# Kernel tuning notes

Hardware: AMD Instinct MI355X
Metric: run time of the kernel (lower is better)

## Reference

```python
import jax, jax.numpy as jnp
import numpy as np
import math

B, C, H, W = 8, 512, 32, 32
NUM_HEADS = 8          # channels // num_head_channels = 512 // 64
NUM_GROUPS = 32        # GroupNorm32
EPS = 1e-5


def setup_inputs() -> dict:
    key = jax.random.key(0)
    k1, k2, k3, k4, k5 = jax.random.split(key, 5)
    x = jax.random.normal(k1, (B, C, H, W), dtype=jnp.float32)
    # GroupNorm affine params (torch init: ones/zeros)
    norm_scale = jnp.ones((C,), dtype=jnp.float32)
    norm_bias = jnp.zeros((C,), dtype=jnp.float32)
    # 1x1 Conv1d weights: qkv maps C -> 3C, proj maps C -> C
    qkv_w = jax.random.normal(k2, (3 * C, C), dtype=jnp.float32) * 0.02
    qkv_b = jax.random.normal(k3, (3 * C,), dtype=jnp.float32) * 0.02
    # NOTE: original zero-inits proj_out; we use small random weights so the
    # block computes non-trivial math (same op structure, same FLOPs).
    proj_w = jax.random.normal(k4, (C, C), dtype=jnp.float32) * 0.02
    proj_b = jax.random.normal(k5, (C,), dtype=jnp.float32) * 0.02
    return {"x": x, "norm_scale": norm_scale, "norm_bias": norm_bias,
            "qkv_w": qkv_w, "qkv_b": qkv_b, "proj_w": proj_w, "proj_b": proj_b}


def _attention_block(x, norm_scale, norm_bias, qkv_w, qkv_b, proj_w, proj_b):
    b, c, h, w = x.shape
    t = h * w
    xf = x.reshape(b, c, t)
    # GroupNorm32: fp32 compute, 32 groups, biased variance, eps=1e-5
    g = xf.astype(jnp.float32).reshape(b, NUM_GROUPS, c // NUM_GROUPS, t)
    mean = g.mean(axis=(2, 3), keepdims=True)
    var = g.var(axis=(2, 3), keepdims=True)
    gn = ((g - mean) * jax.lax.rsqrt(var + EPS)).reshape(b, c, t)
    gn = (gn * norm_scale[None, :, None] + norm_bias[None, :, None]).astype(xf.dtype)
    # 1x1 conv == channel matmul: [B,C,T] -> [B,3C,T]
    qkv = jnp.einsum('oc,bct->bot', qkv_w, gn) + qkv_b[None, :, None]
    # Legacy head layout: [B, H*3*ch, T] -> [B*H, 3*ch, T]
    ch = c // NUM_HEADS
    qkv = qkv.reshape(b * NUM_HEADS, 3 * ch, t)
    q, k, v = jnp.split(qkv, 3, axis=1)          # each [B*H, ch, T]
    scale = 1.0 / math.sqrt(math.sqrt(ch))
    weight = jnp.einsum('bct,bcs->bts', q * scale, k * scale)  # [B*H, T, T]
    weight = jax.nn.softmax(weight.astype(jnp.float32), axis=-1).astype(qkv.dtype)
    a = jnp.einsum('bts,bcs->bct', weight, v).reshape(b, c, t)
    out = jnp.einsum('oc,bct->bot', proj_w, a) + proj_b[None, :, None]
    return (xf + out).reshape(b, c, h, w)


def reference(x, norm_scale, norm_bias, qkv_w, qkv_b, proj_w, proj_b):
    return _attention_block(x, norm_scale, norm_bias, qkv_w, qkv_b, proj_w, proj_b)
```

## Files before the change

kernel.cpp:

```cpp
#include <hip/hip_runtime.h>
#include <math.h>

#define B_   8
#define C_   512
#define T_   1024
#define G_   32
#define CPG  16
#define NH   8
#define OC3  1536
#define EPS  1e-5f

#define QSCALE 0.18033688011112042f
#define C_OFF  11.541560327111708f

typedef __bf16 bf16;
typedef __bf16 bf16x4 __attribute__((ext_vector_type(4)));
typedef __bf16 bf16x8 __attribute__((ext_vector_type(8)));
typedef float  f32x4  __attribute__((ext_vector_type(4)));
typedef short  s16x4  __attribute__((ext_vector_type(4)));

#define MFMA16(a, b, c) __builtin_amdgcn_mfma_f32_16x16x32_bf16((a), (b), (c), 0, 0, 0)

__device__ __forceinline__ f32x4 mfma_k16(bf16x4 a, bf16x4 b, f32x4 c) {
#if __has_builtin(__builtin_amdgcn_mfma_f32_16x16x16_bf16)
    return __builtin_amdgcn_mfma_f32_16x16x16_bf16(a, b, c, 0, 0, 0);
#else
    return __builtin_amdgcn_mfma_f32_16x16x16bf16_1k(
        __builtin_bit_cast(s16x4, a), __builtin_bit_cast(s16x4, b), c, 0, 0, 0);
#endif
}

__device__ __forceinline__ float fexp2(float x) {
#if defined(__has_builtin)
#if __has_builtin(__builtin_amdgcn_exp2f)
    return __builtin_amdgcn_exp2f(x);
#else
    return __expf(x * 0.6931471805599453f);
#endif
#else
    return __expf(x * 0.6931471805599453f);
#endif
}

__global__ __launch_bounds__(256) void cvt_both(const float* __restrict__ w1,
                                                bf16* __restrict__ wb1,
                                                const float* __restrict__ w2,
                                                bf16* __restrict__ wb2)
{
    int blk = blockIdx.x;
    const float* src = (blk < 768) ? w1 : w2;
    bf16* dst        = (blk < 768) ? wb1 : wb2;
    int i = (blk < 768 ? blk : blk - 768) * 256 + threadIdx.x;
    float4 v = ((const float4*)src)[i];
    bf16x4 o;
    o[0] = (bf16)v.x; o[1] = (bf16)v.y; o[2] = (bf16)v.z; o[3] = (bf16)v.w;
    *(bf16x4*)(dst + (size_t)i * 4) = o;
}

__global__ __launch_bounds__(256) void gn_kernel(const float* __restrict__ x,
                                                 const float* __restrict__ scale,
                                                 const float* __restrict__ bias,
                                                 bf16* __restrict__ gnT)
{
    const int blk = blockIdx.x;
    const int b = blk >> 5, g = blk & 31;
    const size_t base = (size_t)blk * (CPG * T_);
    const float4* xin = (const float4*)(x + base);
    const int tid = threadIdx.x;

    float s = 0.f, ss = 0.f;
    float4 vals[16];
#pragma unroll
    for (int i = 0; i < 16; ++i) {
        float4 v = xin[tid + i * 256];
        vals[i] = v;
        s  += v.x + v.y + v.z + v.w;
        ss += v.x * v.x + v.y * v.y + v.z * v.z + v.w * v.w;
    }

    __shared__ float rs[256], rss[256];
    rs[tid] = s; rss[tid] = ss;
    __syncthreads();
    for (int off = 128; off > 0; off >>= 1) {
        if (tid < off) { rs[tid] += rs[tid + off]; rss[tid] += rss[tid + off]; }
        __syncthreads();
    }
    const float invN = 1.f / (float)(CPG * T_);
    const float mean = rs[0] * invN;
    const float var  = rss[0] * invN - mean * mean;
    const float inv  = rsqrtf(var + EPS);

    const int c0 = g * CPG;
    float sc[16], bi[16];
#pragma unroll
    for (int i = 0; i < 16; ++i) {
        float s_ = scale[c0 + i] * inv;
        sc[i] = s_;
        bi[i] = bias[c0 + i] - mean * s_;
    }
    bf16* ob = gnT + (size_t)b * (T_ * C_) + c0;
#pragma unroll
    for (int tt = 0; tt < 4; ++tt) {
        bf16x8 lo, hi;
#pragma unroll
        for (int i = 0; i < 8; ++i) {
            float v0 = (tt == 0) ? vals[i].x : (tt == 1) ? vals[i].y
                     : (tt == 2) ? vals[i].z : vals[i].w;
            float v1 = (tt == 0) ? vals[i + 8].x : (tt == 1) ? vals[i + 8].y
                     : (tt == 2) ? vals[i + 8].z : vals[i + 8].w;
            lo[i] = (bf16)(v0 * sc[i] + bi[i]);
            hi[i] = (bf16)(v1 * sc[i + 8] + bi[i + 8]);
        }
        bf16* p = ob + (size_t)(4 * tid + tt) * C_;
        *(bf16x8*)p       = lo;
        *(bf16x8*)(p + 8) = hi;
    }
}

template <int MODE>
__global__ __launch_bounds__(256) void mm128(const bf16* __restrict__ Arows,
                                             const bf16* __restrict__ Wt,
                                             const float* __restrict__ bias,
                                             const float* __restrict__ x,
                                             void* __restrict__ outp)
{
    const int b   = blockIdx.z;
    const int o0  = blockIdx.y * 128;
    const int t0  = blockIdx.x * 128;
    const int tid = threadIdx.x;
    const int lane = tid & 63;
    const int w  = tid >> 6;
    const int wr = w >> 1, wc = w & 1;
    const int lq = lane & 15, lg = lane >> 4;

    __shared__ __align__(16) bf16 Ag[128][72];
    __shared__ __align__(16) bf16 Bg[128][72];

    const bf16* gA = Arows + (size_t)b * (T_ * C_) + (size_t)t0 * C_;
    const bf16* gB = Wt + (size_t)o0 * C_;

    f32x4 acc[4][4];
#pragma unroll
    for (int i = 0; i < 4; ++i)
#pragma unroll
        for (int j = 0; j < 4; ++j) { acc[i][j][0]=0.f; acc[i][j][1]=0.f; acc[i][j][2]=0.f; acc[i][j][3]=0.f; }

    bf16x8 areg[4], breg[4];
#pragma unroll
    for (int it = 0; it < 4; ++it) {
        int chunk = it * 256 + tid, row = chunk >> 3, cp = chunk & 7;
        areg[it] = *(const bf16x8*)(gA + (size_t)row * C_ + cp * 8);
        breg[it] = *(const bf16x8*)(gB + (size_t)row * C_ + cp * 8);
    }

    for (int k0 = 0; k0 < C_; k0 += 64) {
        __syncthreads();
#pragma unroll
        for (int it = 0; it < 4; ++it) {
            int chunk = it * 256 + tid, row = chunk >> 3, cp = chunk & 7;
            *(bf16x8*)&Ag[row][cp * 8] = areg[it];
            *(bf16x8*)&Bg[row][cp * 8] = breg[it];
        }
        __syncthreads();
        if (k0 + 64 < C_) {
#pragma unroll
            for (int it = 0; it < 4; ++it) {
                int chunk = it * 256 + tid, row = chunk >> 3, cp = chunk & 7;
                areg[it] = *(const bf16x8*)(gA + (size_t)row * C_ + k0 + 64 + cp * 8);
                breg[it] = *(const bf16x8*)(gB + (size_t)row * C_ + k0 + 64 + cp * 8);
            }
        }
#pragma unroll
        for (int kb = 0; kb < 2; ++kb) {
            bf16x8 af[4], bfr[4];
#pragma unroll
            for (int i = 0; i < 4; ++i) {
                af[i]  = *(const bf16x8*)&Ag[wr * 64 + i * 16 + lq][kb * 32 + lg * 8];
                bfr[i] = *(const bf16x8*)&Bg[wc * 64 + i * 16 + lq][kb * 32 + lg * 8];
            }
#pragma unroll
            for (int mf = 0; mf < 4; ++mf)
#pragma unroll
                for (int nf = 0; nf < 4; ++nf)
                    acc[mf][nf] = MFMA16(af[mf], bfr[nf], acc[mf][nf]);
        }
    }

    if (MODE == 0) {
        bf16* qkvT = (bf16*)outp;
#pragma unroll
        for (int nf = 0; nf < 4; ++nf) {
            int chg = o0 + wc * 64 + nf * 16 + lq;
            int seg = chg >> 6;
            int which = seg % 3;
            int chs = chg & 63;
            float bv = bias[chg];
            bf16* outb = qkvT + (size_t)(b * 24 + seg) * (T_ * 64);
            if (which != 2) {
                float osc = (which == 0) ? QSCALE : 1.0f;
#pragma unroll
                for (int mf = 0; mf < 4; ++mf) {
                    int tb = t0 + wr * 64 + mf * 16 + lg * 4;
#pragma unroll
                    for (int r = 0; r < 4; ++r)
                        outb[(size_t)(tb + r) * 64 + chs] = (bf16)((acc[mf][nf][r] + bv) * osc);
                }
            } else {
#pragma unroll
                for (int mf = 0; mf < 4; ++mf) {
                    int tb = t0 + wr * 64 + mf * 16 + lg * 4;
                    bf16x4 pb;
#pragma unroll
                    for (int r = 0; r < 4; ++r) pb[r] = (bf16)(acc[mf][nf][r] + bv);
                    *(bf16x4*)(outb + (size_t)chs * T_ + tb) = pb;
                }
            }
        }
    } else {
        float* out = (float*)outp;
#pragma unroll
        for (int nf = 0; nf < 4; ++nf) {
            int o = o0 + wc * 64 + nf * 16 + lq;
            float bv = bias[o];
#pragma unroll
            for (int mf = 0; mf < 4; ++mf) {
                int tb = t0 + wr * 64 + mf * 16 + lg * 4;
                size_t idx = ((size_t)b * C_ + o) * T_ + tb;
                float4 xr = *(const float4*)(x + idx);
                float4 rv;
                rv.x = acc[mf][nf][0] + bv + xr.x;
                rv.y = acc[mf][nf][1] + bv + xr.y;
                rv.z = acc[mf][nf][2] + bv + xr.z;
                rv.w = acc[mf][nf][3] + bv + xr.w;
                *(float4*)(out + idx) = rv;
            }
        }
    }
}

__global__ __launch_bounds__(256) void attn_kernel(const bf16* __restrict__ qkvT,
                                                   bf16* __restrict__ aT)
{
    const int id = blockIdx.x;
    const int bh = id & 63;
    const int tile = id >> 6;
    const int tid = threadIdx.x;
    const int lane = tid & 63;
    const int w  = tid >> 6;
    const int lq = lane & 15;
    const int lg = lane >> 4;
    const int q0 = tile * 128 + w * 32;

    const bf16* qb = qkvT + (size_t)(bh * 3 + 0) * (T_ * 64);
    const bf16* kb = qkvT + (size_t)(bh * 3 + 1) * (T_ * 64);
    const bf16* vb = qkvT + (size_t)(bh * 3 + 2) * (T_ * 64);

    __shared__ __align__(16) bf16 ks[64][72];
    __shared__ __align__(16) bf16 vs[64][136];

    bf16x8 qf[2][2];
#pragma unroll
    for (int qg = 0; qg < 2; ++qg)
#pragma unroll
        for (int kh = 0; kh < 2; ++kh)
            qf[qg][kh] = *(const bf16x8*)(qb + (size_t)(q0 + qg * 16 + lq) * 64 + kh * 32 + lg * 8);

    f32x4 oacc[2][4];
#pragma unroll
    for (int qg = 0; qg < 2; ++qg)
#pragma unroll
        for (int og = 0; og < 4; ++og) { oacc[qg][og][0]=0.f; oacc[qg][og][1]=0.f; oacc[qg][og][2]=0.f; oacc[qg][og][3]=0.f; }
    float lloc[2] = {0.f, 0.f};

    const int sr = tid >> 3, scp = tid & 7;
    bf16x8 kreg[2], vreg[2];
#pragma unroll
    for (int it = 0; it < 2; ++it) {
        kreg[it] = *(const bf16x8*)(kb + (size_t)(sr + it * 32) * 64 + scp * 8);
        vreg[it] = *(const bf16x8*)(vb + (size_t)(sr + it * 32) * T_ + scp * 8);
    }

    for (int s0 = 0; s0 < T_; s0 += 64) {
        __syncthreads();
#pragma unroll
        for (int it = 0; it < 2; ++it) {
            *(bf16x8*)&ks[sr + it * 32][scp * 8] = kreg[it];
            *(bf16x8*)&vs[sr + it * 32][scp * 8] = vreg[it];
        }
        __syncthreads();
        if (s0 + 64 < T_) {
            int sn = s0 + 64;
#pragma unroll
            for (int it = 0; it < 2; ++it) {
                kreg[it] = *(const bf16x8*)(kb + (size_t)(sn + sr + it * 32) * 64 + scp * 8);
                vreg[it] = *(const bf16x8*)(vb + (size_t)(sr + it * 32) * T_ + sn + scp * 8);
            }
        }

        f32x4 st[2][4];
        f32x4 cinit; cinit[0] = -C_OFF; cinit[1] = -C_OFF; cinit[2] = -C_OFF; cinit[3] = -C_OFF;
#pragma unroll
        for (int g = 0; g < 4; ++g) {
            bf16x8 kf0 = *(const bf16x8*)&ks[g * 16 + lq][lg * 8];
            bf16x8 kf1 = *(const bf16x8*)&ks[g * 16 + lq][32 + lg * 8];
#pragma unroll
            for (int qg = 0; qg < 2; ++qg) {
                st[qg][g] = MFMA16(kf0, qf[qg][0], cinit);
                st[qg][g] = MFMA16(kf1, qf[qg][1], st[qg][g]);
            }
        }
        bf16x4 pa16[2][4];
#pragma unroll
        for (int qg = 0; qg < 2; ++qg) {
            float ll = 0.f;
#pragma unroll
            for (int g = 0; g < 4; ++g) {
#pragma unroll
                for (int r = 0; r < 4; ++r) {
                    float p = fexp2(st[qg][g][r]);
                    ll += p;
                    pa16[qg][g][r] = (bf16)p;
                }
            }
            lloc[qg] += ll;
        }
#pragma unroll
        for (int og = 0; og < 4; ++og) {
#pragma unroll
            for (int g = 0; g < 4; ++g) {
                bf16x4 vf = *(const bf16x4*)&vs[og * 16 + lq][g * 16 + lg * 4];
#pragma unroll
                for (int qg = 0; qg < 2; ++qg)
                    oacc[qg][og] = mfma_k16(pa16[qg][g], vf, oacc[qg][og]);
            }
        }
    }

    const int b = bh >> 3, h = bh & 7;
#pragma unroll
    for (int qg = 0; qg < 2; ++qg) {
        float l = lloc[qg];
        l += __shfl_xor(l, 16);
        l += __shfl_xor(l, 32);
        float linv = 1.f / l;
        float li[4];
#pragma unroll
        for (int r = 0; r < 4; ++r) li[r] = __shfl(linv, lg * 4 + r);
        bf16* ob = aT + ((size_t)b * T_ + q0 + qg * 16 + lg * 4) * C_ + h * 64 + lq;
#pragma unroll
        for (int og = 0; og < 4; ++og)
#pragma unroll
            for (int r = 0; r < 4; ++r)
                ob[(size_t)r * C_ + og * 16] = (bf16)(oacc[qg][og][r] * li[r]);
    }
}

extern "C" void kernel_launch(void* const* d_in, const int* in_sizes, int n_in,
                              void* d_out, int out_size, void* d_ws, size_t ws_size,
                              hipStream_t stream)
{
    (void)in_sizes; (void)n_in; (void)out_size; (void)ws_size;
    const float* x      = (const float*)d_in[0];
    const float* nscale = (const float*)d_in[1];
    const float* nbias  = (const float*)d_in[2];
    const float* qkv_w  = (const float*)d_in[3];
    const float* qkv_b  = (const float*)d_in[4];
    const float* proj_w = (const float*)d_in[5];
    const float* proj_b = (const float*)d_in[6];
    float* out = (float*)d_out;

    char* wsb = (char*)d_ws;
    bf16*  gnT  = (bf16*) (wsb);
    bf16*  Wb   = (bf16*) (wsb + (size_t)(8  << 20));
    bf16*  PWb  = Wb + (size_t)OC3 * C_;
    bf16*  qkvT = (bf16*) (wsb + (size_t)(12 << 20));
    bf16*  aT   = (bf16*) (wsb + (size_t)(36 << 20));

    cvt_both<<<1024, 256, 0, stream>>>(qkv_w, Wb, proj_w, PWb);
    gn_kernel<<<B_ * G_, 256, 0, stream>>>(x, nscale, nbias, gnT);
    mm128<0><<<dim3(T_ / 128, OC3 / 128, B_), 256, 0, stream>>>(gnT, Wb, qkv_b, nullptr, qkvT);
    attn_kernel<<<512, 256, 0, stream>>>(qkvT, aT);
    mm128<1><<<dim3(T_ / 128, C_ / 128, B_), 256, 0, stream>>>(aT, PWb, proj_b, x, out);
}
```

Baseline: 82.82 us.

## Double-buffer attention K/V tiles, MFMA row sums, stage QK stores through LDS

The attention kernel now double-buffers the K/V shared-memory tiles, so each iteration needs one barrier instead of two and the next tile's LDS writes overlap compute. Softmax row sums are computed with an MFMA against a ones vector, which removes the scalar accumulation and the cross-lane shuffles. It also raises wave priority around the MFMA sections. The QKV projection stages its Q/K outputs through LDS so they go to global memory as coalesced 16-byte row writes instead of scattered 2-byte stores, at the cost of extra LDS and a barrier.

Result: slower. 84.52 us (+2.0%).

```diff
diff --git a/kernel.cpp b/kernel.cpp
--- a/kernel.cpp
+++ b/kernel.cpp
@@ -133,8 +133,9 @@
     const int wr = w >> 1, wc = w & 1;
     const int lq = lane & 15, lg = lane >> 4;
 
-    __shared__ __align__(16) bf16 Ag[128][72];
-    __shared__ __align__(16) bf16 Bg[128][72];
+    __shared__ __align__(16) bf16 smem_raw[2 * 128 * 72];
+    bf16 (*Ag)[72] = (bf16(*)[72])smem_raw;
+    bf16 (*Bg)[72] = (bf16(*)[72])(smem_raw + 128 * 72);
 
     const bf16* gA = Arows + (size_t)b * (T_ * C_) + (size_t)t0 * C_;
     const bf16* gB = Wt + (size_t)o0 * C_;
@@ -188,32 +189,49 @@
 
     if (MODE == 0) {
         bf16* qkvT = (bf16*)outp;
+        bf16* tb = smem_raw;
+        __syncthreads();
 #pragma unroll
         for (int nf = 0; nf < 4; ++nf) {
-            int chg = o0 + wc * 64 + nf * 16 + lq;
+            int chl = wc * 64 + nf * 16 + lq;
+            int chg = o0 + chl;
             int seg = chg >> 6;
             int which = seg % 3;
             int chs = chg & 63;
             float bv = bias[chg];
-            bf16* outb = qkvT + (size_t)(b * 24 + seg) * (T_ * 64);
             if (which != 2) {
                 float osc = (which == 0) ? QSCALE : 1.0f;
 #pragma unroll
                 for (int mf = 0; mf < 4; ++mf) {
-                    int tb = t0 + wr * 64 + mf * 16 + lg * 4;
+                    int tl = wr * 64 + mf * 16 + lg * 4;
 #pragma unroll
                     for (int r = 0; r < 4; ++r)
-                        outb[(size_t)(tb + r) * 64 + chs] = (bf16)((acc[mf][nf][r] + bv) * osc);
+                        tb[(tl + r) * 136 + chl] = (bf16)((acc[mf][nf][r] + bv) * osc);
                 }
             } else {
+                bf16* outb = qkvT + (size_t)(b * 24 + seg) * (T_ * 64);
 #pragma unroll
                 for (int mf = 0; mf < 4; ++mf) {
-                    int tb = t0 + wr * 64 + mf * 16 + lg * 4;
+                    int tbi = t0 + wr * 64 + mf * 16 + lg * 4;
                     bf16x4 pb;
 #pragma unroll
                     for (int r = 0; r < 4; ++r) pb[r] = (bf16)(acc[mf][nf][r] + bv);
-                    *(bf16x4*)(outb + (size_t)chs * T_ + tb) = pb;
+                    *(bf16x4*)(outb + (size_t)chs * T_ + tbi) = pb;
                 }
+            }
+        }
+        __syncthreads();
+#pragma unroll
+        for (int sh = 0; sh < 2; ++sh) {
+            int seg = (o0 >> 6) + sh;
+            if (seg % 3 == 2) continue;
+            bf16* outb = qkvT + (size_t)(b * 24 + seg) * (T_ * 64);
+#pragma unroll
+            for (int it = 0; it < 4; ++it) {
+                int chunk = it * 256 + tid;
+                int t = chunk >> 3, c = (chunk & 7) * 8;
+                bf16x8 v = *(const bf16x8*)&tb[t * 136 + sh * 64 + c];
+                *(bf16x8*)(outb + (size_t)(t0 + t) * 64 + c) = v;
             }
         }
     } else {
@@ -224,8 +242,8 @@
             float bv = bias[o];
 #pragma unroll
             for (int mf = 0; mf < 4; ++mf) {
-                int tb = t0 + wr * 64 + mf * 16 + lg * 4;
-                size_t idx = ((size_t)b * C_ + o) * T_ + tb;
+                int tbi = t0 + wr * 64 + mf * 16 + lg * 4;
+                size_t idx = ((size_t)b * C_ + o) * T_ + tbi;
                 float4 xr = *(const float4*)(x + idx);
                 float4 rv;
                 rv.x = acc[mf][nf][0] + bv + xr.x;
@@ -255,8 +273,8 @@
     const bf16* kb = qkvT + (size_t)(bh * 3 + 1) * (T_ * 64);
     const bf16* vb = qkvT + (size_t)(bh * 3 + 2) * (T_ * 64);
 
-    __shared__ __align__(16) bf16 ks[64][72];
-    __shared__ __align__(16) bf16 vs[64][136];
+    __shared__ __align__(16) bf16 ks[2][64][72];
+    __shared__ __align__(16) bf16 vs[2][64][136];
 
     bf16x8 qf[2][2];
 #pragma unroll
@@ -265,12 +283,16 @@
         for (int kh = 0; kh < 2; ++kh)
             qf[qg][kh] = *(const bf16x8*)(qb + (size_t)(q0 + qg * 16 + lq) * 64 + kh * 32 + lg * 8);
 
-    f32x4 oacc[2][4];
-#pragma unroll
-    for (int qg = 0; qg < 2; ++qg)
+    f32x4 oacc[2][4], lacc[2];
+#pragma unroll
+    for (int qg = 0; qg < 2; ++qg) {
+        lacc[qg][0]=0.f; lacc[qg][1]=0.f; lacc[qg][2]=0.f; lacc[qg][3]=0.f;
 #pragma unroll
         for (int og = 0; og < 4; ++og) { oacc[qg][og][0]=0.f; oacc[qg][og][1]=0.f; oacc[qg][og][2]=0.f; oacc[qg][og][3]=0.f; }
-    float lloc[2] = {0.f, 0.f};
+    }
+
+    bf16x4 vones;
+    vones[0] = (bf16)1.0f; vones[1] = (bf16)1.0f; vones[2] = (bf16)1.0f; vones[3] = (bf16)1.0f;
 
     const int sr = tid >> 3, scp = tid & 7;
     bf16x8 kreg[2], vreg[2];
@@ -279,17 +301,29 @@
         kreg[it] = *(const bf16x8*)(kb + (size_t)(sr + it * 32) * 64 + scp * 8);
         vreg[it] = *(const bf16x8*)(vb + (size_t)(sr + it * 32) * T_ + scp * 8);
     }
-
-    for (int s0 = 0; s0 < T_; s0 += 64) {
-        __syncthreads();
-#pragma unroll
-        for (int it = 0; it < 2; ++it) {
-            *(bf16x8*)&ks[sr + it * 32][scp * 8] = kreg[it];
-            *(bf16x8*)&vs[sr + it * 32][scp * 8] = vreg[it];
-        }
-        __syncthreads();
-        if (s0 + 64 < T_) {
-            int sn = s0 + 64;
+#pragma unroll
+    for (int it = 0; it < 2; ++it) {
+        *(bf16x8*)&ks[0][sr + it * 32][scp * 8] = kreg[it];
+        *(bf16x8*)&vs[0][sr + it * 32][scp * 8] = vreg[it];
+    }
+#pragma unroll
+    for (int it = 0; it < 2; ++it) {
+        kreg[it] = *(const bf16x8*)(kb + (size_t)(64 + sr + it * 32) * 64 + scp * 8);
+        vreg[it] = *(const bf16x8*)(vb + (size_t)(sr + it * 32) * T_ + 64 + scp * 8);
+    }
+    __syncthreads();
+
+    for (int i = 0; i < 16; ++i) {
+        const int cur = i & 1;
+        if (i < 15) {
+#pragma unroll
+            for (int it = 0; it < 2; ++it) {
+                *(bf16x8*)&ks[cur ^ 1][sr + it * 32][scp * 8] = kreg[it];
+                *(bf16x8*)&vs[cur ^ 1][sr + it * 32][scp * 8] = vreg[it];
+            }
+        }
+        if (i < 14) {
+            int sn = (i + 2) * 64;
 #pragma unroll
             for (int it = 0; it < 2; ++it) {
                 kreg[it] = *(const bf16x8*)(kb + (size_t)(sn + sr + it * 32) * 64 + scp * 8);
@@ -299,53 +333,52 @@
 
         f32x4 st[2][4];
         f32x4 cinit; cinit[0] = -C_OFF; cinit[1] = -C_OFF; cinit[2] = -C_OFF; cinit[3] = -C_OFF;
+        __builtin_amdgcn_s_setprio(1);
 #pragma unroll
         for (int g = 0; g < 4; ++g) {
-            bf16x8 kf0 = *(const bf16x8*)&ks[g * 16 + lq][lg * 8];
-            bf16x8 kf1 = *(const bf16x8*)&ks[g * 16 + lq][32 + lg * 8];
+            bf16x8 kf0 = *(const bf16x8*)&ks[cur][g * 16 + lq][lg * 8];
+            bf16x8 kf1 = *(const bf16x8*)&ks[cur][g * 16 + lq][32 + lg * 8];
 #pragma unroll
             for (int qg = 0; qg < 2; ++qg) {
                 st[qg][g] = MFMA16(kf0, qf[qg][0], cinit);
                 st[qg][g] = MFMA16(kf1, qf[qg][1], st[qg][g]);
             }
         }
+        __builtin_amdgcn_s_setprio(0);
         bf16x4 pa16[2][4];
 #pragma unroll
-        for (int qg = 0; qg < 2; ++qg) {
-            float ll = 0.f;
+        for (int qg = 0; qg < 2; ++qg)
+#pragma unroll
+            for (int g = 0; g < 4; ++g)
+#pragma unroll
+                for (int r = 0; r < 4; ++r)
+                    pa16[qg][g][r] = (bf16)fexp2(st[qg][g][r]);
+        __builtin_amdgcn_s_setprio(1);
+#pragma unroll
+        for (int qg = 0; qg < 2; ++qg)
+#pragma unroll
+            for (int g = 0; g < 4; ++g)
+                lacc[qg] = mfma_k16(pa16[qg][g], vones, lacc[qg]);
+#pragma unroll
+        for (int og = 0; og < 4; ++og) {
 #pragma unroll
             for (int g = 0; g < 4; ++g) {
-#pragma unroll
-                for (int r = 0; r < 4; ++r) {
-                    float p = fexp2(st[qg][g][r]);
-                    ll += p;
-                    pa16[qg][g][r] = (bf16)p;
-                }
-            }
-            lloc[qg] += ll;
-        }
-#pragma unroll
-        for (int og = 0; og < 4; ++og) {
-#pragma unroll
-            for (int g = 0; g < 4; ++g) {
-                bf16x4 vf = *(const bf16x4*)&vs[og * 16 + lq][g * 16 + lg * 4];
+                bf16x4 vf = *(const bf16x4*)&vs[cur][og * 16 + lq][g * 16 + lg * 4];
 #pragma unroll
                 for (int qg = 0; qg < 2; ++qg)
                     oacc[qg][og] = mfma_k16(pa16[qg][g], vf, oacc[qg][og]);
             }
         }
+        __builtin_amdgcn_s_setprio(0);
+        __syncthreads();
     }
 
     const int b = bh >> 3, h = bh & 7;
 #pragma unroll
     for (int qg = 0; qg < 2; ++qg) {
-        float l = lloc[qg];
-        l += __shfl_xor(l, 16);
-        l += __shfl_xor(l, 32);
-        float linv = 1.f / l;
         float li[4];
 #pragma unroll
-        for (int r = 0; r < 4; ++r) li[r] = __shfl(linv, lg * 4 + r);
+        for (int r = 0; r < 4; ++r) li[r] = 1.f / lacc[qg][r];
         bf16* ob = aT + ((size_t)b * T_ + q0 + qg * 16 + lg * 4) * C_ + h * 64 + lq;
 #pragma unroll
         for (int og = 0; og < 4; ++og)
```

## Halve attention query tile per block and compute row sums via MFMA

Applied to the files above, without the earlier changes.

Each attention block now handles 64 queries instead of 128, with each wave owning 16 query rows, and the grid doubles to 1024 blocks to give more parallelism and lower register use per wave. The softmax denominator is now accumulated with an extra MFMA against a vector of ones instead of scalar adds plus cross-lane shuffles. In exchange, K/V tiles are loaded from global memory and staged into LDS twice as often per query, and the row sums are taken from the bf16-rounded probabilities.

Result: slower. 86.74 us (+4.7%).

```diff
diff --git a/kernel.cpp b/kernel.cpp
--- a/kernel.cpp
+++ b/kernel.cpp
@@ -249,7 +249,7 @@
     const int w  = tid >> 6;
     const int lq = lane & 15;
     const int lg = lane >> 4;
-    const int q0 = tile * 128 + w * 32;
+    const int q0 = tile * 64 + w * 16;
 
     const bf16* qb = qkvT + (size_t)(bh * 3 + 0) * (T_ * 64);
     const bf16* kb = qkvT + (size_t)(bh * 3 + 1) * (T_ * 64);
@@ -258,19 +258,18 @@
     __shared__ __align__(16) bf16 ks[64][72];
     __shared__ __align__(16) bf16 vs[64][136];
 
-    bf16x8 qf[2][2];
-#pragma unroll
-    for (int qg = 0; qg < 2; ++qg)
-#pragma unroll
-        for (int kh = 0; kh < 2; ++kh)
-            qf[qg][kh] = *(const bf16x8*)(qb + (size_t)(q0 + qg * 16 + lq) * 64 + kh * 32 + lg * 8);
-
-    f32x4 oacc[2][4];
-#pragma unroll
-    for (int qg = 0; qg < 2; ++qg)
-#pragma unroll
-        for (int og = 0; og < 4; ++og) { oacc[qg][og][0]=0.f; oacc[qg][og][1]=0.f; oacc[qg][og][2]=0.f; oacc[qg][og][3]=0.f; }
-    float lloc[2] = {0.f, 0.f};
+    bf16x8 qf[2];
+#pragma unroll
+    for (int kh = 0; kh < 2; ++kh)
+        qf[kh] = *(const bf16x8*)(qb + (size_t)(q0 + lq) * 64 + kh * 32 + lg * 8);
+
+    f32x4 oacc[4], lacc;
+    lacc[0]=0.f; lacc[1]=0.f; lacc[2]=0.f; lacc[3]=0.f;
+#pragma unroll
+    for (int og = 0; og < 4; ++og) { oacc[og][0]=0.f; oacc[og][1]=0.f; oacc[og][2]=0.f; oacc[og][3]=0.f; }
+
+    bf16x4 vones;
+    vones[0] = (bf16)1.0f; vones[1] = (bf16)1.0f; vones[2] = (bf16)1.0f; vones[3] = (bf16)1.0f;
 
     const int sr = tid >> 3, scp = tid & 7;
     bf16x8 kreg[2], vreg[2];
@@ -280,7 +279,7 @@
         vreg[it] = *(const bf16x8*)(vb + (size_t)(sr + it * 32) * T_ + scp * 8);
     }
 
-    for (int s0 = 0; s0 < T_; s0 += 64) {
+    for (int i = 0; i < 16; ++i) {
         __syncthreads();
 #pragma unroll
         for (int it = 0; it < 2; ++it) {
@@ -288,8 +287,8 @@
             *(bf16x8*)&vs[sr + it * 32][scp * 8] = vreg[it];
         }
         __syncthreads();
-        if (s0 + 64 < T_) {
-            int sn = s0 + 64;
+        if (i < 15) {
+            int sn = (i + 1) * 64;
 #pragma unroll
             for (int it = 0; it < 2; ++it) {
                 kreg[it] = *(const bf16x8*)(kb + (size_t)(sn + sr + it * 32) * 64 + scp * 8);
@@ -297,62 +296,44 @@
             }
         }
 
-        f32x4 st[2][4];
+        f32x4 st[4];
         f32x4 cinit; cinit[0] = -C_OFF; cinit[1] = -C_OFF; cinit[2] = -C_OFF; cinit[3] = -C_OFF;
 #pragma unroll
         for (int g = 0; g < 4; ++g) {
             bf16x8 kf0 = *(const bf16x8*)&ks[g * 16 + lq][lg * 8];
             bf16x8 kf1 = *(const bf16x8*)&ks[g * 16 + lq][32 + lg * 8];
-#pragma unroll
-            for (int qg = 0; qg < 2; ++qg) {
-                st[qg][g] = MFMA16(kf0, qf[qg][0], cinit);
-                st[qg][g] = MFMA16(kf1, qf[qg][1], st[qg][g]);
-            }
-        }
-        bf16x4 pa16[2][4];
-#pragma unroll
-        for (int qg = 0; qg < 2; ++qg) {
-            float ll = 0.f;
-#pragma unroll
-            for (int g = 0; g < 4; ++g) {
-#pragma unroll
-                for (int r = 0; r < 4; ++r) {
-                    float p = fexp2(st[qg][g][r]);
-                    ll += p;
-                    pa16[qg][g][r] = (bf16)p;
-                }
-            }
-            lloc[qg] += ll;
-        }
+            st[g] = MFMA16(kf0, qf[0], cinit);
+            st[g] = MFMA16(kf1, qf[1], st[g]);
+        }
+        bf16x4 pa16[4];
+#pragma unroll
+        for (int g = 0; g < 4; ++g)
+#pragma unroll
+            for (int r = 0; r < 4; ++r)
+                pa16[g][r] = (bf16)fexp2(st[g][r]);
+#pragma unroll
+        for (int g = 0; g < 4; ++g)
+            lacc = mfma_k16(pa16[g], vones, lacc);
 #pragma unroll
         for (int og = 0; og < 4; ++og) {
 #pragma unroll
             for (int g = 0; g < 4; ++g) {
                 bf16x4 vf = *(const bf16x4*)&vs[og * 16 + lq][g * 16 + lg * 4];
-#pragma unroll
-                for (int qg = 0; qg < 2; ++qg)
-                    oacc[qg][og] = mfma_k16(pa16[qg][g], vf, oacc[qg][og]);
+                oacc[og] = mfma_k16(pa16[g], vf, oacc[og]);
             }
         }
     }
 
     const int b = bh >> 3, h = bh & 7;
-#pragma unroll
-    for (int qg = 0; qg < 2; ++qg) {
-        float l = lloc[qg];
-        l += __shfl_xor(l, 16);
-        l += __shfl_xor(l, 32);
-        float linv = 1.f / l;
-        float li[4];
-#pragma unroll
-        for (int r = 0; r < 4; ++r) li[r] = __shfl(linv, lg * 4 + r);
-        bf16* ob = aT + ((size_t)b * T_ + q0 + qg * 16 + lg * 4) * C_ + h * 64 + lq;
-#pragma unroll
-        for (int og = 0; og < 4; ++og)
-#pragma unroll
-            for (int r = 0; r < 4; ++r)
-                ob[(size_t)r * C_ + og * 16] = (bf16)(oacc[qg][og][r] * li[r]);
-    }
+    float li[4];
+#pragma unroll
+    for (int r = 0; r < 4; ++r) li[r] = 1.f / lacc[r];
+    bf16* ob = aT + ((size_t)b * T_ + q0 + lg * 4) * C_ + h * 64 + lq;
+#pragma unroll
+    for (int og = 0; og < 4; ++og)
+#pragma unroll
+        for (int r = 0; r < 4; ++r)
+            ob[(size_t)r * C_ + og * 16] = (bf16)(oacc[og][r] * li[r]);
 }
 
 extern "C" void kernel_launch(void* const* d_in, const int* in_sizes, int n_in,
@@ -379,6 +360,6 @@
     cvt_both<<<1024, 256, 0, stream>>>(qkv_w, Wb, proj_w, PWb);
     gn_kernel<<<B_ * G_, 256, 0, stream>>>(x, nscale, nbias, gnT);
     mm128<0><<<dim3(T_ / 128, OC3 / 128, B_), 256, 0, stream>>>(gnT, Wb, qkv_b, nullptr, qkvT);
-    attn_kernel<<<512, 256, 0, stream>>>(qkvT, aT);
+    attn_kernel<<<1024, 256, 0, stream>>>(qkvT, aT);
     mm128<1><<<dim3(T_ / 128, C_ / 128, B_), 256, 0, stream>>>(aT, PWb, proj_b, x, out);
 }
```
